# Performance work log

Measured on AMD Instinct MI355X. Metric: run time of the kernel, lower is better.

## Reference

```python
import jax, jax.numpy as jnp
import numpy as np

B, S, H, I, E, K = 2, 2048, 1024, 2048, 8, 2


def setup_inputs() -> dict:
    key = jax.random.key(0)
    k1, k2, k3, k4, k5 = jax.random.split(key, 5)
    scale_h = 1.0 / np.sqrt(H)
    scale_i = 1.0 / np.sqrt(I)
    return {
        "x": jax.random.normal(k1, (B, S, H), dtype=jnp.float32),
        "Wg": jax.random.normal(k2, (H, E), dtype=jnp.float32) * scale_h,
        "W11": jax.random.normal(k3, (E, H, I), dtype=jnp.float32) * scale_h,
        "W12": jax.random.normal(k4, (E, H, I), dtype=jnp.float32) * scale_h,
        "W2": jax.random.normal(k5, (E, I, H), dtype=jnp.float32) * scale_i,
    }


def reference(x, Wg, W11, W12, W2):
    # Router: softmax over experts, then top-k with renormalization (+1e-8 as in torch ref)
    gate_scores = jax.nn.softmax(x @ Wg, axis=-1)          # [B,S,E]
    topk_scores, topk_idx = jax.lax.top_k(gate_scores, K)   # [B,S,K]
    topk_scores = topk_scores / (topk_scores.sum(-1, keepdims=True) + 1e-8)

    # Dense per-expert SwiGLU on all tokens (matches reference's masked-dense math)
    gate = jnp.einsum('bsh,ehi->bsei', x, W11)              # [B,S,E,I]
    value = jnp.einsum('bsh,ehi->bsei', x, W12)
    fused = (gate * jax.nn.sigmoid(gate)) * value           # SiLU(gate) * value
    expert_out = jnp.einsum('bsei,eih->bseh', fused, W2)    # [B,S,E,H]

    # Gather the top-k experts' outputs per token and combine with routing weights
    gathered = jnp.take_along_axis(expert_out, topk_idx[..., None], axis=2)  # [B,S,K,H]
    out = jnp.sum(topk_scores[..., None] * gathered, axis=2)                 # [B,S,H]
    return out
```

## Files before the change

### kernel.cpp

```cpp
#include <hip/hip_runtime.h>
#include <hip/hip_bf16.h>
#include <stdint.h>

#define B_ 2
#define S_ 2048
#define H_ 1024
#define I_ 2048
#define E_ 8
#define TOK (B_*S_)
#define PAIRS (TOK*2)
#define MAXBLK 80

typedef __bf16 bf16_t;
typedef __bf16 bf16x4 __attribute__((ext_vector_type(4)));
typedef __bf16 bf16x8 __attribute__((ext_vector_type(8)));
typedef float  f32x4  __attribute__((ext_vector_type(4)));
typedef float  f32x16 __attribute__((ext_vector_type(16)));

__device__ __forceinline__ void gl_lds16(const bf16_t* g, bf16_t* l) {
    __builtin_amdgcn_global_load_lds(
        (const __attribute__((address_space(1))) unsigned int*)g,
        (__attribute__((address_space(3))) unsigned int*)l, 16, 0, 0);
}

__device__ __forceinline__ void cfence() { asm volatile("" ::: "memory"); }

__global__ void router_kernel(const float* __restrict__ x, const float* __restrict__ Wg,
                              int* __restrict__ top2e, float* __restrict__ top2w,
                              int* __restrict__ counts, bf16_t* __restrict__ xb) {
    int wave = threadIdx.x >> 6;
    int lane = threadIdx.x & 63;
    int t = blockIdx.x * 4 + wave;
    if (t >= TOK) return;
    float acc[E_];
#pragma unroll
    for (int e = 0; e < E_; e++) acc[e] = 0.f;
    const float* xrow = x + (size_t)t * H_;
    for (int j = 0; j < H_ / 64; j++) {
        int h = j * 64 + lane;
        float xv = xrow[h];
        const float4* wg = (const float4*)(Wg + (size_t)h * E_);
        float4 w0 = wg[0], w1 = wg[1];
        acc[0] += xv * w0.x; acc[1] += xv * w0.y; acc[2] += xv * w0.z; acc[3] += xv * w0.w;
        acc[4] += xv * w1.x; acc[5] += xv * w1.y; acc[6] += xv * w1.z; acc[7] += xv * w1.w;
    }
#pragma unroll
    for (int part = 0; part < 2; part++) {
        int idx = part * 512 + lane * 8;
        float4 v0 = *(const float4*)(xrow + idx);
        float4 v1 = *(const float4*)(xrow + idx + 4);
        bf16x8 ov = { (bf16_t)v0.x, (bf16_t)v0.y, (bf16_t)v0.z, (bf16_t)v0.w,
                      (bf16_t)v1.x, (bf16_t)v1.y, (bf16_t)v1.z, (bf16_t)v1.w };
        *(bf16x8*)(xb + (size_t)t * H_ + idx) = ov;
    }
#pragma unroll
    for (int e = 0; e < E_; e++) {
#pragma unroll
        for (int m = 32; m >= 1; m >>= 1) acc[e] += __shfl_xor(acc[e], m, 64);
    }
    if (lane == 0) {
        float mx = acc[0];
        for (int e = 1; e < E_; e++) mx = fmaxf(mx, acc[e]);
        float p[E_]; float z = 0.f;
        for (int e = 0; e < E_; e++) { p[e] = __expf(acc[e] - mx); z += p[e]; }
        for (int e = 0; e < E_; e++) p[e] /= z;
        int i1 = 0; float p1 = p[0];
        for (int e = 1; e < E_; e++) if (p[e] > p1) { p1 = p[e]; i1 = e; }
        int i2 = -1; float p2 = -1.f;
        for (int e = 0; e < E_; e++) if (e != i1 && p[e] > p2) { p2 = p[e]; i2 = e; }
        float s = p1 + p2 + 1e-8f;
        top2e[t * 2]     = i1; top2e[t * 2 + 1] = i2;
        top2w[t * 2]     = p1 / s; top2w[t * 2 + 1] = p2 / s;
        atomicAdd(&counts[i1], 1);
        atomicAdd(&counts[i2], 1);
    }
}

__global__ __launch_bounds__(256) void scanfill_kernel(
    const int* __restrict__ counts, int* __restrict__ offsets,
    int* __restrict__ blk_e, int* __restrict__ blk_m0, int* __restrict__ nblk,
    const int* __restrict__ top2e, int* __restrict__ pair_tok, int* __restrict__ inv) {
    __shared__ int s_cur[E_];
    if (threadIdx.x == 0) {
        int run = 0, b = 0;
        for (int e = 0; e < E_; e++) {
            offsets[e] = run; s_cur[e] = run;
            int c = counts[e];
            for (int m0 = 0; m0 < c; m0 += 128) { blk_e[b] = e; blk_m0[b] = m0; b++; }
            run += c;
        }
        nblk[0] = b;
    }
    __syncthreads();
    for (int p = threadIdx.x; p < PAIRS; p += 256) {
        int e = top2e[p];
        int pos = atomicAdd(&s_cur[e], 1);
        pair_tok[pos] = p >> 1;
        inv[p] = pos;
    }
}

__global__ __launch_bounds__(256) void wtrans_kernel(
    const float* __restrict__ W11, const float* __restrict__ W12,
    const float* __restrict__ W2,
    bf16_t* __restrict__ W11t, bf16_t* __restrict__ W12t, bf16_t* __restrict__ W2t) {
    __shared__ float tile[64][129];
    int z = blockIdx.y;
    int wsel = z >> 3, e = z & 7;
    const float* sbase; bf16_t* dbase; int R, C, tx, ty;
    if (wsel == 0)      { sbase = W11; dbase = W11t; R = H_; C = I_; }
    else if (wsel == 1) { sbase = W12; dbase = W12t; R = H_; C = I_; }
    else                { sbase = W2;  dbase = W2t;  R = I_; C = H_; }
    if (wsel < 2) { tx = blockIdx.x & 15; ty = blockIdx.x >> 4; }
    else          { tx = blockIdx.x & 7;  ty = blockIdx.x >> 3; }
    const float* s = sbase + (size_t)e * R * C;
    bf16_t* d = dbase + (size_t)e * R * C;
    int c0 = tx * 128, r0 = ty * 64;
    int t = threadIdx.x;
#pragma unroll
    for (int j = 0; j < 8; j++) {
        int flat = j * 256 + t;
        int r = flat >> 5;
        int c4 = (flat & 31) * 4;
        float4 v = *(const float4*)(s + (size_t)(r0 + r) * C + c0 + c4);
        tile[r][c4 + 0] = v.x;
        tile[r][c4 + 1] = v.y;
        tile[r][c4 + 2] = v.z;
        tile[r][c4 + 3] = v.w;
    }
    __syncthreads();
#pragma unroll
    for (int j = 0; j < 4; j++) {
        int flat = j * 256 + t;
        int orow = flat >> 3;
        int seg  = (flat & 7) * 8;
        bf16x8 v;
#pragma unroll
        for (int k = 0; k < 8; k++) v[k] = (bf16_t)tile[seg + k][orow];
        *(bf16x8*)(d + (size_t)(c0 + orow) * R + r0 + seg) = v;
    }
}

__global__ __launch_bounds__(256, 2) void gemm1_kernel(
    const bf16_t* __restrict__ xb,
    const bf16_t* __restrict__ W11t,
    const bf16_t* __restrict__ W12t,
    const int* __restrict__ counts, const int* __restrict__ offsets,
    const int* __restrict__ blk_e, const int* __restrict__ blk_m0,
    const int* __restrict__ nblk,
    const int* __restrict__ pair_tok,
    bf16_t* __restrict__ fused)
{
    int by = blockIdx.y;
    if (by >= nblk[0]) return;
    int e = blk_e[by];
    int m0 = blk_m0[by];
    int cnt = counts[e];
    int off = offsets[e];
    int n0 = blockIdx.x * 128;

    __shared__ __align__(16) bf16_t la[2][128 * 32];
    __shared__ __align__(16) bf16_t lb[2][256 * 32];

    int tid = threadIdx.x;
    int w = tid >> 6, lane = tid & 63;
    int wm = w >> 1, wn = w & 1;
    int lrow4 = lane >> 2;
    int lcol4 = lane & 3;
    int sch   = lcol4 ^ (lrow4 & 3);
    int r32 = lane & 31, khalf = lane >> 5;

    const bf16_t* aptr[2];
    const bf16_t* bptr[4];
#pragma unroll
    for (int it = 0; it < 2; it++) {
        int r = it * 64 + w * 16 + lrow4;
        int grow = m0 + r;
        int tok = pair_tok[off + (grow < cnt ? grow : 0)];
        aptr[it] = xb + (size_t)tok * H_ + sch * 8;
    }
#pragma unroll
    for (int it = 0; it < 4; it++) {
        int r = it * 64 + w * 16 + lrow4;
        const bf16_t* base = (r < 128)
            ? (W11t + ((size_t)e * I_ + n0 + r) * H_)
            : (W12t + ((size_t)e * I_ + n0 + (r - 128)) * H_);
        bptr[it] = base + sch * 8;
    }

    f32x16 acc[2][4];
#pragma unroll
    for (int a = 0; a < 2; a++)
#pragma unroll
        for (int b = 0; b < 4; b++) acc[a][b] = (f32x16)(0.f);

#pragma unroll
    for (int it = 0; it < 2; it++) gl_lds16(aptr[it], &la[0][(it * 64 + w * 16) * 32]);
#pragma unroll
    for (int it = 0; it < 4; it++) gl_lds16(bptr[it], &lb[0][(it * 64 + w * 16) * 32]);

    const int NT = H_ / 32;
    for (int t = 0; t < NT; t++) {
        int cur = t & 1;
        if (t + 1 < NT) {
            int nxt = cur ^ 1;
            int ko = (t + 1) * 32;
#pragma unroll
            for (int it = 0; it < 2; it++) gl_lds16(aptr[it] + ko, &la[nxt][(it * 64 + w * 16) * 32]);
#pragma unroll
            for (int it = 0; it < 4; it++) gl_lds16(bptr[it] + ko, &lb[nxt][(it * 64 + w * 16) * 32]);
            asm volatile("s_waitcnt vmcnt(6)" ::: "memory");
        } else {
            asm volatile("s_waitcnt vmcnt(0)" ::: "memory");
        }
        __builtin_amdgcn_s_barrier();
        __builtin_amdgcn_sched_barrier(0);
        cfence();

        const bf16_t* A = la[cur];
        const bf16_t* Bb = lb[cur];
#pragma unroll
        for (int t16 = 0; t16 < 2; t16++) {
            int seg = t16 * 2 + khalf;
            bf16x8 af[2], bfr[4];
#pragma unroll
            for (int ms = 0; ms < 2; ms++) {
                int row = wm * 64 + ms * 32 + r32;
                af[ms] = *(const bf16x8*)&A[row * 32 + (seg ^ (r32 & 3)) * 8];
            }
#pragma unroll
            for (int ns = 0; ns < 2; ns++) {
                int browg = wn * 64 + ns * 32 + r32;
                bfr[ns]     = *(const bf16x8*)&Bb[browg * 32 + (seg ^ (r32 & 3)) * 8];
                bfr[ns + 2] = *(const bf16x8*)&Bb[(browg + 128) * 32 + (seg ^ (r32 & 3)) * 8];
            }
#pragma unroll
            for (int ms = 0; ms < 2; ms++)
#pragma unroll
                for (int ns = 0; ns < 4; ns++)
                    acc[ms][ns] = __builtin_amdgcn_mfma_f32_32x32x16_bf16(
                        af[ms], bfr[ns], acc[ms][ns], 0, 0, 0);
        }
        asm volatile("s_waitcnt lgkmcnt(0)" ::: "memory");
        __builtin_amdgcn_sched_barrier(0);
        __builtin_amdgcn_s_barrier();
        cfence();
    }

#pragma unroll
    for (int ms = 0; ms < 2; ms++) {
#pragma unroll
        for (int ns = 0; ns < 2; ns++) {
            int i = n0 + wn * 64 + ns * 32 + r32;
#pragma unroll
            for (int reg = 0; reg < 16; reg++) {
                int rrow = (reg & 3) + 8 * (reg >> 2) + 4 * khalf;
                int grow = m0 + wm * 64 + ms * 32 + rrow;
                if (grow < cnt) {
                    float g = acc[ms][ns][reg];
                    float v = acc[ms][ns + 2][reg];
                    float f = g * v / (1.f + __expf(-g));
                    fused[(size_t)(off + grow) * I_ + i] = (bf16_t)f;
                }
            }
        }
    }
}

__global__ __launch_bounds__(256, 3) void gemm2_kernel(
    const bf16_t* __restrict__ fused,
    const bf16_t* __restrict__ W2t,
    const int* __restrict__ counts, const int* __restrict__ offsets,
    const int* __restrict__ blk_e, const int* __restrict__ blk_m0,
    const int* __restrict__ nblk,
    bf16_t* __restrict__ y)
{
    int by = blockIdx.y;
    if (by >= nblk[0]) return;
    int e = blk_e[by];
    int m0 = blk_m0[by];
    int cnt = counts[e];
    int off = offsets[e];
    int n0 = blockIdx.x * 128;

    __shared__ __align__(16) bf16_t la[2][128 * 32];
    __shared__ __align__(16) bf16_t lb[2][128 * 32];

    int tid = threadIdx.x;
    int w = tid >> 6, lane = tid & 63;
    int wm = w >> 1, wn = w & 1;
    int lrow4 = lane >> 2;
    int lcol4 = lane & 3;
    int sch   = lcol4 ^ (lrow4 & 3);
    int r32 = lane & 31, khalf = lane >> 5;

    const bf16_t* aptr[2];
    const bf16_t* bptr[2];
#pragma unroll
    for (int it = 0; it < 2; it++) {
        int r = it * 64 + w * 16 + lrow4;
        int grow = m0 + r;
        if (grow >= cnt) grow = cnt - 1;
        aptr[it] = fused + (size_t)(off + grow) * I_ + sch * 8;
        bptr[it] = W2t + ((size_t)e * H_ + n0 + r) * I_ + sch * 8;
    }

    f32x16 acc[2][2];
#pragma unroll
    for (int a = 0; a < 2; a++)
#pragma unroll
        for (int b = 0; b < 2; b++) acc[a][b] = (f32x16)(0.f);

#pragma unroll
    for (int it = 0; it < 2; it++) {
        gl_lds16(aptr[it], &la[0][(it * 64 + w * 16) * 32]);
        gl_lds16(bptr[it], &lb[0][(it * 64 + w * 16) * 32]);
    }

    const int NT = I_ / 32;
    for (int t = 0; t < NT; t++) {
        int cur = t & 1;
        if (t + 1 < NT) {
            int nxt = cur ^ 1;
            int ko = (t + 1) * 32;
#pragma unroll
            for (int it = 0; it < 2; it++) {
                gl_lds16(aptr[it] + ko, &la[nxt][(it * 64 + w * 16) * 32]);
                gl_lds16(bptr[it] + ko, &lb[nxt][(it * 64 + w * 16) * 32]);
            }
            asm volatile("s_waitcnt vmcnt(4)" ::: "memory");
        } else {
            asm volatile("s_waitcnt vmcnt(0)" ::: "memory");
        }
        __builtin_amdgcn_s_barrier();
        __builtin_amdgcn_sched_barrier(0);
        cfence();

        const bf16_t* A = la[cur];
        const bf16_t* Bb = lb[cur];
#pragma unroll
        for (int t16 = 0; t16 < 2; t16++) {
            int seg = t16 * 2 + khalf;
            bf16x8 af[2], bfr[2];
#pragma unroll
            for (int ms = 0; ms < 2; ms++) {
                int row = wm * 64 + ms * 32 + r32;
                af[ms] = *(const bf16x8*)&A[row * 32 + (seg ^ (r32 & 3)) * 8];
            }
#pragma unroll
            for (int ns = 0; ns < 2; ns++) {
                int brow = wn * 64 + ns * 32 + r32;
                bfr[ns] = *(const bf16x8*)&Bb[brow * 32 + (seg ^ (r32 & 3)) * 8];
            }
#pragma unroll
            for (int ms = 0; ms < 2; ms++)
#pragma unroll
                for (int ns = 0; ns < 2; ns++)
                    acc[ms][ns] = __builtin_amdgcn_mfma_f32_32x32x16_bf16(
                        af[ms], bfr[ns], acc[ms][ns], 0, 0, 0);
        }
        asm volatile("s_waitcnt lgkmcnt(0)" ::: "memory");
        __builtin_amdgcn_sched_barrier(0);
        __builtin_amdgcn_s_barrier();
        cfence();
    }

#pragma unroll
    for (int ms = 0; ms < 2; ms++) {
#pragma unroll
        for (int reg = 0; reg < 16; reg++) {
            int rrow = (reg & 3) + 8 * (reg >> 2) + 4 * khalf;
            int grow = m0 + wm * 64 + ms * 32 + rrow;
            if (grow < cnt) {
                int slot = off + grow;
#pragma unroll
                for (int ns = 0; ns < 2; ns++) {
                    int h = n0 + wn * 64 + ns * 32 + r32;
                    y[(size_t)slot * H_ + h] = (bf16_t)acc[ms][ns][reg];
                }
            }
        }
    }
}

__global__ __launch_bounds__(256) void combine_kernel(
    const bf16_t* __restrict__ y, const int* __restrict__ inv,
    const float* __restrict__ top2w, float* __restrict__ out) {
    int t = blockIdx.x;
    int h = threadIdx.x * 4;
    int s1 = inv[t * 2], s2 = inv[t * 2 + 1];
    float w1 = top2w[t * 2], w2 = top2w[t * 2 + 1];
    bf16x4 a = *(const bf16x4*)(y + (size_t)s1 * H_ + h);
    bf16x4 b = *(const bf16x4*)(y + (size_t)s2 * H_ + h);
    f32x4 r;
#pragma unroll
    for (int k = 0; k < 4; k++) r[k] = w1 * (float)a[k] + w2 * (float)b[k];
    *(f32x4*)(out + (size_t)t * H_ + h) = r;
}

extern "C" void kernel_launch(void* const* d_in, const int* in_sizes, int n_in,
                              void* d_out, int out_size, void* d_ws, size_t ws_size,
                              hipStream_t stream) {
    const float* x   = (const float*)d_in[0];
    const float* Wg  = (const float*)d_in[1];
    const float* W11 = (const float*)d_in[2];
    const float* W12 = (const float*)d_in[3];
    const float* W2  = (const float*)d_in[4];
    float* out = (float*)d_out;

    char* ws = (char*)d_ws;
    size_t o = 0;
    auto alloc = [&](size_t bytes) { size_t r = o; o = (o + bytes + 255) & ~(size_t)255; return r; };
    int*    counts   = (int*)(ws + alloc(E_ * 4));
    int*    offsets  = (int*)(ws + alloc(E_ * 4));
    int*    blk_e    = (int*)(ws + alloc(MAXBLK * 4));
    int*    blk_m0   = (int*)(ws + alloc(MAXBLK * 4));
    int*    nblk     = (int*)(ws + alloc(4));
    int*    top2e    = (int*)(ws + alloc(TOK * 2 * 4));
    float*  top2w    = (float*)(ws + alloc(TOK * 2 * 4));
    int*    pair_tok = (int*)(ws + alloc(PAIRS * 4));
    int*    inv      = (int*)(ws + alloc(TOK * 2 * 4));
    bf16_t* xb       = (bf16_t*)(ws + alloc((size_t)TOK * H_ * 2));
    bf16_t* W11t     = (bf16_t*)(ws + alloc((size_t)E_ * I_ * H_ * 2));
    bf16_t* W12t     = (bf16_t*)(ws + alloc((size_t)E_ * I_ * H_ * 2));
    bf16_t* W2t      = (bf16_t*)(ws + alloc((size_t)E_ * I_ * H_ * 2));
    bf16_t* fusedbuf = (bf16_t*)(ws + alloc((size_t)PAIRS * I_ * 2));
    bf16_t* ybuf     = (bf16_t*)(ws + alloc((size_t)PAIRS * H_ * 2));

    hipMemsetAsync(counts, 0, E_ * 4, stream);

    router_kernel<<<TOK / 4, 256, 0, stream>>>(x, Wg, top2e, top2w, counts, xb);
    scanfill_kernel<<<1, 256, 0, stream>>>(counts, offsets, blk_e, blk_m0, nblk,
                                           top2e, pair_tok, inv);
    wtrans_kernel<<<dim3(256, 24), 256, 0, stream>>>(W11, W12, W2, W11t, W12t, W2t);

    gemm1_kernel<<<dim3(I_ / 128, MAXBLK), 256, 0, stream>>>(
        xb, W11t, W12t, counts, offsets, blk_e, blk_m0, nblk, pair_tok, fusedbuf);
    gemm2_kernel<<<dim3(H_ / 128, MAXBLK), 256, 0, stream>>>(
        fusedbuf, W2t, counts, offsets, blk_e, blk_m0, nblk, ybuf);
    combine_kernel<<<TOK, 256, 0, stream>>>(ybuf, inv, top2w, out);
}
```

Measured before the change: 537.6 us.

## Triple-buffer LDS tiles with one barrier per k-step and new XOR swizzle

Both expert GEMM kernels move from double- to triple-buffered LDS staging. Loads are issued two k-tiles ahead, and the two barriers per iteration collapse to one placed after compute. This is meant to hide more global-load latency and cut synchronisation per step. The LDS swizzle also changes from row&3 to (row>>1)&3 to reduce bank conflicts on the 16-byte fragment reads. In exchange, LDS use per block rises by half (gemm1 to 144KB for two blocks), which may limit occupancy under the launch bounds.

```diff
diff --git a/kernel.cpp b/kernel.cpp
--- a/kernel.cpp
+++ b/kernel.cpp
@@ -159,16 +159,17 @@
     int off = offsets[e];
     int n0 = blockIdx.x * 128;
 
-    __shared__ __align__(16) bf16_t la[2][128 * 32];
-    __shared__ __align__(16) bf16_t lb[2][256 * 32];
+    __shared__ __align__(16) bf16_t la[3][128 * 32];
+    __shared__ __align__(16) bf16_t lb[3][256 * 32];
 
     int tid = threadIdx.x;
     int w = tid >> 6, lane = tid & 63;
     int wm = w >> 1, wn = w & 1;
     int lrow4 = lane >> 2;
     int lcol4 = lane & 3;
-    int sch   = lcol4 ^ (lrow4 & 3);
+    int sch   = lcol4 ^ ((lrow4 >> 1) & 3);
     int r32 = lane & 31, khalf = lane >> 5;
+    int rsw = (r32 >> 1) & 3;
 
     const bf16_t* aptr[2];
     const bf16_t* bptr[4];
@@ -198,27 +199,29 @@
     for (int it = 0; it < 2; it++) gl_lds16(aptr[it], &la[0][(it * 64 + w * 16) * 32]);
 #pragma unroll
     for (int it = 0; it < 4; it++) gl_lds16(bptr[it], &lb[0][(it * 64 + w * 16) * 32]);
+#pragma unroll
+    for (int it = 0; it < 2; it++) gl_lds16(aptr[it] + 32, &la[1][(it * 64 + w * 16) * 32]);
+#pragma unroll
+    for (int it = 0; it < 4; it++) gl_lds16(bptr[it] + 32, &lb[1][(it * 64 + w * 16) * 32]);
+    asm volatile("s_waitcnt vmcnt(6)" ::: "memory");
+    __builtin_amdgcn_s_barrier();
+    __builtin_amdgcn_sched_barrier(0);
+    cfence();
 
     const int NT = H_ / 32;
+    int bcur = 0;
     for (int t = 0; t < NT; t++) {
-        int cur = t & 1;
-        if (t + 1 < NT) {
-            int nxt = cur ^ 1;
-            int ko = (t + 1) * 32;
-#pragma unroll
-            for (int it = 0; it < 2; it++) gl_lds16(aptr[it] + ko, &la[nxt][(it * 64 + w * 16) * 32]);
-#pragma unroll
-            for (int it = 0; it < 4; it++) gl_lds16(bptr[it] + ko, &lb[nxt][(it * 64 + w * 16) * 32]);
-            asm volatile("s_waitcnt vmcnt(6)" ::: "memory");
-        } else {
-            asm volatile("s_waitcnt vmcnt(0)" ::: "memory");
-        }
-        __builtin_amdgcn_s_barrier();
-        __builtin_amdgcn_sched_barrier(0);
-        cfence();
-
-        const bf16_t* A = la[cur];
-        const bf16_t* Bb = lb[cur];
+        if (t + 2 < NT) {
+            int bnxt = bcur + 2; if (bnxt >= 3) bnxt -= 3;
+            int ko = (t + 2) * 32;
+#pragma unroll
+            for (int it = 0; it < 2; it++) gl_lds16(aptr[it] + ko, &la[bnxt][(it * 64 + w * 16) * 32]);
+#pragma unroll
+            for (int it = 0; it < 4; it++) gl_lds16(bptr[it] + ko, &lb[bnxt][(it * 64 + w * 16) * 32]);
+        }
+
+        const bf16_t* A = la[bcur];
+        const bf16_t* Bb = lb[bcur];
 #pragma unroll
         for (int t16 = 0; t16 < 2; t16++) {
             int seg = t16 * 2 + khalf;
@@ -226,13 +229,13 @@
 #pragma unroll
             for (int ms = 0; ms < 2; ms++) {
                 int row = wm * 64 + ms * 32 + r32;
-                af[ms] = *(const bf16x8*)&A[row * 32 + (seg ^ (r32 & 3)) * 8];
+                af[ms] = *(const bf16x8*)&A[row * 32 + (seg ^ rsw) * 8];
             }
 #pragma unroll
             for (int ns = 0; ns < 2; ns++) {
                 int browg = wn * 64 + ns * 32 + r32;
-                bfr[ns]     = *(const bf16x8*)&Bb[browg * 32 + (seg ^ (r32 & 3)) * 8];
-                bfr[ns + 2] = *(const bf16x8*)&Bb[(browg + 128) * 32 + (seg ^ (r32 & 3)) * 8];
+                bfr[ns]     = *(const bf16x8*)&Bb[browg * 32 + (seg ^ rsw) * 8];
+                bfr[ns + 2] = *(const bf16x8*)&Bb[(browg + 128) * 32 + (seg ^ rsw) * 8];
             }
 #pragma unroll
             for (int ms = 0; ms < 2; ms++)
@@ -242,9 +245,12 @@
                         af[ms], bfr[ns], acc[ms][ns], 0, 0, 0);
         }
         asm volatile("s_waitcnt lgkmcnt(0)" ::: "memory");
+        if (t + 2 < NT) { asm volatile("s_waitcnt vmcnt(6)" ::: "memory"); }
+        else            { asm volatile("s_waitcnt vmcnt(0)" ::: "memory"); }
         __builtin_amdgcn_sched_barrier(0);
         __builtin_amdgcn_s_barrier();
         cfence();
+        bcur++; if (bcur >= 3) bcur = 0;
     }
 
 #pragma unroll
@@ -283,16 +289,17 @@
     int off = offsets[e];
     int n0 = blockIdx.x * 128;
 
-    __shared__ __align__(16) bf16_t la[2][128 * 32];
-    __shared__ __align__(16) bf16_t lb[2][128 * 32];
+    __shared__ __align__(16) bf16_t la[3][128 * 32];
+    __shared__ __align__(16) bf16_t lb[3][128 * 32];
 
     int tid = threadIdx.x;
     int w = tid >> 6, lane = tid & 63;
     int wm = w >> 1, wn = w & 1;
     int lrow4 = lane >> 2;
     int lcol4 = lane & 3;
-    int sch   = lcol4 ^ (lrow4 & 3);
+    int sch   = lcol4 ^ ((lrow4 >> 1) & 3);
     int r32 = lane & 31, khalf = lane >> 5;
+    int rsw = (r32 >> 1) & 3;
 
     const bf16_t* aptr[2];
     const bf16_t* bptr[2];
@@ -316,28 +323,31 @@
         gl_lds16(aptr[it], &la[0][(it * 64 + w * 16) * 32]);
         gl_lds16(bptr[it], &lb[0][(it * 64 + w * 16) * 32]);
     }
+#pragma unroll
+    for (int it = 0; it < 2; it++) {
+        gl_lds16(aptr[it] + 32, &la[1][(it * 64 + w * 16) * 32]);
+        gl_lds16(bptr[it] + 32, &lb[1][(it * 64 + w * 16) * 32]);
+    }
+    asm volatile("s_waitcnt vmcnt(4)" ::: "memory");
+    __builtin_amdgcn_s_barrier();
+    __builtin_amdgcn_sched_barrier(0);
+    cfence();
 
     const int NT = I_ / 32;
+    int bcur = 0;
     for (int t = 0; t < NT; t++) {
-        int cur = t & 1;
-        if (t + 1 < NT) {
-            int nxt = cur ^ 1;
-            int ko = (t + 1) * 32;
+        if (t + 2 < NT) {
+            int bnxt = bcur + 2; if (bnxt >= 3) bnxt -= 3;
+            int ko = (t + 2) * 32;
 #pragma unroll
             for (int it = 0; it < 2; it++) {
-                gl_lds16(aptr[it] + ko, &la[nxt][(it * 64 + w * 16) * 32]);
-                gl_lds16(bptr[it] + ko, &lb[nxt][(it * 64 + w * 16) * 32]);
-            }
-            asm volatile("s_waitcnt vmcnt(4)" ::: "memory");
-        } else {
-            asm volatile("s_waitcnt vmcnt(0)" ::: "memory");
-        }
-        __builtin_amdgcn_s_barrier();
-        __builtin_amdgcn_sched_barrier(0);
-        cfence();
-
-        const bf16_t* A = la[cur];
-        const bf16_t* Bb = lb[cur];
+                gl_lds16(aptr[it] + ko, &la[bnxt][(it * 64 + w * 16) * 32]);
+                gl_lds16(bptr[it] + ko, &lb[bnxt][(it * 64 + w * 16) * 32]);
+            }
+        }
+
+        const bf16_t* A = la[bcur];
+        const bf16_t* Bb = lb[bcur];
 #pragma unroll
         for (int t16 = 0; t16 < 2; t16++) {
             int seg = t16 * 2 + khalf;
@@ -345,12 +355,12 @@
 #pragma unroll
             for (int ms = 0; ms < 2; ms++) {
                 int row = wm * 64 + ms * 32 + r32;
-                af[ms] = *(const bf16x8*)&A[row * 32 + (seg ^ (r32 & 3)) * 8];
+                af[ms] = *(const bf16x8*)&A[row * 32 + (seg ^ rsw) * 8];
             }
 #pragma unroll
             for (int ns = 0; ns < 2; ns++) {
                 int brow = wn * 64 + ns * 32 + r32;
-                bfr[ns] = *(const bf16x8*)&Bb[brow * 32 + (seg ^ (r32 & 3)) * 8];
+                bfr[ns] = *(const bf16x8*)&Bb[brow * 32 + (seg ^ rsw) * 8];
             }
 #pragma unroll
             for (int ms = 0; ms < 2; ms++)
@@ -360,9 +370,12 @@
                         af[ms], bfr[ns], acc[ms][ns], 0, 0, 0);
         }
         asm volatile("s_waitcnt lgkmcnt(0)" ::: "memory");
+        if (t + 2 < NT) { asm volatile("s_waitcnt vmcnt(4)" ::: "memory"); }
+        else            { asm volatile("s_waitcnt vmcnt(0)" ::: "memory"); }
         __builtin_amdgcn_sched_barrier(0);
         __builtin_amdgcn_s_barrier();
         cfence();
+        bcur++; if (bcur >= 3) bcur = 0;
     }
 
 #pragma unroll
```

After: 522.5 us. 1.03x faster.
